# Optimization experiments

Measured on AMD Instinct MI355X. Metric: run time of the kernel, lower is better.

## Reference

```python
import jax, jax.numpy as jnp
import numpy as np

EPS = 1e-06


def _feature_map(x):
    # elu(x) + 1  (elu with alpha=1)
    return jnp.where(x > 0, x + 1.0, jnp.exp(x))


def setup_inputs() -> dict:
    key = jax.random.key(0)
    k1, k2, k3 = jax.random.split(key, 3)
    N, L, S, H, D = 4, 8192, 8192, 8, 64
    q = jax.random.normal(k1, (N, L, H, D), dtype=jnp.float32)
    k = jax.random.normal(k2, (N, S, H, D), dtype=jnp.float32)
    v = jax.random.normal(k3, (N, S, H, D), dtype=jnp.float32)
    q_mask = jnp.ones((N, L), dtype=jnp.float32)
    kv_mask = jnp.ones((N, S), dtype=jnp.float32)
    return {"q": q, "k": k, "v": v, "q_mask": q_mask, "kv_mask": kv_mask}


def reference(q, k, v, q_mask, kv_mask):
    # Linear attention with elu+1 feature map (Katharopoulos et al.)
    qf = _feature_map(q)  # [N, L, H, D]
    kf = _feature_map(k)  # [N, S, H, D]
    qf = q_mask[:, :, None, None] * qf
    kf = kv_mask[:, :, None, None] * kf
    vm = kv_mask[:, :, None, None] * v
    S = v.shape[1]
    # global KV state: [N, H, D, Dv]; v scaled by 1/S for numerical stability
    kv = jnp.einsum('nshd,nshv->nhdv', kf, vm / S)
    # normalizer: einsum('nlhd,nshd->nlh') == q . sum_s(k)
    k_sum = kf.sum(axis=1)  # [N, H, D]
    div = 1.0 / (jnp.einsum('nlhd,nhd->nlh', qf, k_sum) + EPS)
    out = S * jnp.einsum('nlhd,nhdv,nlh->nlhv', qf, kv, div)
    return out
```

## Files before the change

kernel.cpp:

```cpp
#include <hip/hip_runtime.h>
#include <math.h>


#define EPS 1e-6f

static constexpr int Nc = 4;
static constexpr int Lc = 8192;
static constexpr int Sc = 8192;
static constexpr int Hc = 8;
static constexpr int NH = Nc * Hc;
static constexpr int STATE = 64 * 64 + 64;
static constexpr int TS = 32;
static constexpr int TSP = 36;
static constexpr int QSP = 68;

typedef __attribute__((ext_vector_type(4))) short short4v;
typedef __attribute__((ext_vector_type(8))) short short8v;
typedef __attribute__((ext_vector_type(4))) float f32x4;

__device__ __forceinline__ float fmap(float x) {
    return x > 0.f ? x + 1.f : __expf(x);
}
__device__ __forceinline__ unsigned short f2bf(float x) {
    unsigned int u = __float_as_uint(x);
    u += 0x7FFFu + ((u >> 16) & 1u);
    return (unsigned short)(u >> 16);
}
__device__ __forceinline__ float bf2f(unsigned short h) {
    return __uint_as_float(((unsigned int)h) << 16);
}
__device__ __forceinline__ short8v ld8(const unsigned short* p) {
    short4v a = *(const short4v*)p;
    short4v b = *(const short4v*)(p + 4);
    return __builtin_shufflevector(a, b, 0, 1, 2, 3, 4, 5, 6, 7);
}
__device__ __forceinline__ unsigned int pack2(unsigned short a, unsigned short b) {
    return (unsigned)a | ((unsigned)b << 16);
}

__global__ __launch_bounds__(256, 4) void k1_partial(
    const float* __restrict__ kg, const float* __restrict__ vg,
    const float* __restrict__ kv_mask,
    float* __restrict__ partial, int chunks, int sc)
{
    __shared__ unsigned short kTh[64][TSP], kTl[64][TSP];
    __shared__ unsigned short vTh[64][TSP], vTl[64][TSP];
    __shared__ float ksb[16][64];

    const int bid = blockIdx.x;
    const int pair = bid / chunks;
    const int chunk = bid - pair * chunks;
    const int n = pair >> 3;
    const int h = pair & 7;
    const int s0 = chunk * sc;
    const int t = threadIdx.x;
    const int g = t >> 4;
    const int c4 = (t & 15) * 4;
    const int lane = t & 63;
    const int wv = t >> 6;
    const int row16 = lane & 15;
    const int g8 = (lane >> 4) * 8;

    f32x4 acc[4] = {{0.f,0.f,0.f,0.f},{0.f,0.f,0.f,0.f},
                    {0.f,0.f,0.f,0.f},{0.f,0.f,0.f,0.f}};
    float ksm[4] = {0.f, 0.f, 0.f, 0.f};

    const size_t rowstride = (size_t)Hc * 64;
    const size_t gbase = ((size_t)n * Sc * Hc + h) * 64 + c4;
    const int mbase = n * Sc;

    auto issue = [&](int sbase, float4& a0, float4& a1, float4& b0, float4& b1,
                     float& me, float& mo) {
        const int s = s0 + sbase + 2 * g;
        const size_t be = gbase + (size_t)s * rowstride;
        a0 = *(const float4*)(kg + be);
        a1 = *(const float4*)(kg + be + rowstride);
        b0 = *(const float4*)(vg + be);
        b1 = *(const float4*)(vg + be + rowstride);
        me = kv_mask[mbase + s];
        mo = kv_mask[mbase + s + 1];
    };

    auto process = [&](const float4& ck0, const float4& ck1,
                       const float4& cv0, const float4& cv1,
                       float cme, float cmo) {
        const float* kep = &ck0.x;
        const float* kop = &ck1.x;
        const float* vep = &cv0.x;
        const float* vop = &cv1.x;
        #pragma unroll
        for (int j = 0; j < 4; ++j) {
            const float fe = cme * fmap(kep[j]);
            const float fo = cmo * fmap(kop[j]);
            ksm[j] += fe + fo;
            const unsigned short he = f2bf(fe), ho = f2bf(fo);
            const unsigned short le = f2bf(fe - bf2f(he)), lo_ = f2bf(fo - bf2f(ho));
            *(unsigned int*)&kTh[c4 + j][2 * g] = pack2(he, ho);
            *(unsigned int*)&kTl[c4 + j][2 * g] = pack2(le, lo_);
            const float ue = cme * vep[j];
            const float uo = cmo * vop[j];
            const unsigned short vhe = f2bf(ue), vho = f2bf(uo);
            const unsigned short vle = f2bf(ue - bf2f(vhe)), vlo = f2bf(uo - bf2f(vho));
            *(unsigned int*)&vTh[c4 + j][2 * g] = pack2(vhe, vho);
            *(unsigned int*)&vTl[c4 + j][2 * g] = pack2(vle, vlo);
        }
        __syncthreads();

        const short8v Ah = ld8(&kTh[wv * 16 + row16][g8]);
        const short8v Al = ld8(&kTl[wv * 16 + row16][g8]);
        #pragma unroll
        for (int bt = 0; bt < 4; ++bt) {
            const short8v Bh = ld8(&vTh[bt * 16 + row16][g8]);
            const short8v Bl = ld8(&vTl[bt * 16 + row16][g8]);
            acc[bt] = __builtin_amdgcn_mfma_f32_16x16x32_bf16(Ah, Bh, acc[bt], 0, 0, 0);
            acc[bt] = __builtin_amdgcn_mfma_f32_16x16x32_bf16(Al, Bh, acc[bt], 0, 0, 0);
            acc[bt] = __builtin_amdgcn_mfma_f32_16x16x32_bf16(Ah, Bl, acc[bt], 0, 0, 0);
        }
        __syncthreads();
    };

    float4 ka0, ka1, va0, va1, kb0, kb1, vb0, vb1;
    float mea, moa, meb, mob;

    issue(0, ka0, ka1, va0, va1, mea, moa);
    for (int sb = 0; sb < sc; sb += 2 * TS) {
        issue(sb + TS, kb0, kb1, vb0, vb1, meb, mob);
        process(ka0, ka1, va0, va1, mea, moa);
        const int na = (sb + 2 * TS < sc) ? sb + 2 * TS : sb;
        issue(na, ka0, ka1, va0, va1, mea, moa);
        process(kb0, kb1, vb0, vb1, meb, mob);
    }

    float* outp = partial + (size_t)bid * STATE;
    float (*outs)[QSP] = reinterpret_cast<float (*)[QSP]>(&kTh[0][0]);
    #pragma unroll
    for (int bt = 0; bt < 4; ++bt) {
        #pragma unroll
        for (int r = 0; r < 4; ++r) {
            const int row = wv * 16 + (lane >> 4) * 4 + r;
            outs[row][bt * 16 + row16] = acc[bt][r];
        }
    }
    __syncthreads();
    #pragma unroll
    for (int p = 0; p < 4; ++p) {
        const int f = t + p * 256;
        const int row = f >> 4;
        const int cc = (f & 15) * 4;
        *(float4*)(outp + row * 64 + cc) = *(const float4*)&outs[row][cc];
    }

    *(f32x4*)&ksb[g][c4] = (f32x4){ksm[0], ksm[1], ksm[2], ksm[3]};
    __syncthreads();
    if (t < 64) {
        float s = 0.f;
        #pragma unroll
        for (int i = 0; i < 16; ++i) s += ksb[i][t];
        outp[4096 + t] = s;
    }
}

__global__ __launch_bounds__(256) void k2c_reduce_finalize(
    const float* __restrict__ src, float* __restrict__ dst, int nred)
{
    const int b = blockIdx.x;
    const int pair = b >> 1;
    const int sub = b & 1;
    const int t = threadIdx.x;
    const int ep = sub * 256 + t;
    const int d0 = (ep >> 4) * 2;
    const int c4 = (ep & 15) * 4;

    const float* sbase = src + (size_t)pair * nred * STATE;
    f32x4 a0 = {0.f,0.f,0.f,0.f}, a1 = {0.f,0.f,0.f,0.f};
    #pragma unroll 4
    for (int j = 0; j < nred; ++j) {
        const float* pj = sbase + (size_t)j * STATE;
        a0 += *(const f32x4*)(pj + (size_t)d0 * 64 + c4);
        a1 += *(const f32x4*)(pj + (size_t)(d0 + 1) * 64 + c4);
    }

    unsigned int* dw = (unsigned int*)(dst + (size_t)pair * STATE);
    #pragma unroll
    for (int i = 0; i < 4; ++i) {
        const int w = (c4 + i) * 32 + (d0 >> 1);
        const unsigned short h0 = f2bf(a0[i]), h1 = f2bf(a1[i]);
        dw[w] = pack2(h0, h1);
        dw[2048 + w] = pack2(f2bf(a0[i] - bf2f(h0)), f2bf(a1[i] - bf2f(h1)));
    }

    if (sub == 0 && t < 16) {
        f32x4 a = {0.f,0.f,0.f,0.f};
        #pragma unroll 4
        for (int j = 0; j < nred; ++j)
            a += *(const f32x4*)(sbase + (size_t)j * STATE + 4096 + t * 4);
        *(f32x4*)(dst + (size_t)pair * STATE + 4096 + t * 4) = a;
    }
}

__global__ __launch_bounds__(256, 4) void k3_out(
    const float* __restrict__ qg, const float* __restrict__ state,
    const float* __restrict__ q_mask, float* __restrict__ outg)
{
    __shared__ __align__(16) unsigned short qsp[2][64][QSP];
    __shared__ unsigned short kvt[2][64][QSP];
    __shared__ float ksum[64];
    __shared__ float dinv[64];

    const int nblk = 64;
    const int bid = blockIdx.x;
    const int pair = bid / nblk;
    const int lb = (bid - pair * nblk) * 2;
    const int n = pair >> 3;
    const int h = pair & 7;
    const int t = threadIdx.x;
    const int lane = t & 63;
    const int wv = t >> 6;
    const int row16 = lane & 15;
    const int g8 = (lane >> 4) * 8;

    const unsigned int* sw = (const unsigned int*)(state + (size_t)pair * STATE);
    #pragma unroll
    for (int i = 0; i < 8; ++i) {
        const int w = t + i * 256;
        const int dv = w >> 5;
        const int d2 = (w & 31) * 2;
        *(unsigned int*)&kvt[0][dv][d2] = sw[w];
        *(unsigned int*)&kvt[1][dv][d2] = sw[2048 + w];
    }
    if (t < 64) ksum[t] = ((const float*)state)[(size_t)pair * STATE + 4096 + t];
    __syncthreads();

    for (int tl = 0; tl < 2; ++tl) {
        const int l0 = (lb + tl) * 64;

        #pragma unroll
        for (int p = 0; p < 4; ++p) {
            const int f = t + p * 256;
            const int row = f >> 4;
            const int c4 = (f & 15) * 4;
            const int l = l0 + row;
            const size_t base = ((size_t)(n * Lc + l) * Hc + h) * 64 + c4;
            const float4 qq = *(const float4*)(qg + base);
            const float m = q_mask[n * Lc + l];
            const float q0 = m * fmap(qq.x), q1 = m * fmap(qq.y);
            const float q2 = m * fmap(qq.z), q3 = m * fmap(qq.w);
            const unsigned short h0 = f2bf(q0), h1 = f2bf(q1), h2 = f2bf(q2), h3 = f2bf(q3);
            *(unsigned int*)&qsp[0][row][c4]     = pack2(h0, h1);
            *(unsigned int*)&qsp[0][row][c4 + 2] = pack2(h2, h3);
            *(unsigned int*)&qsp[1][row][c4]     = pack2(f2bf(q0 - bf2f(h0)), f2bf(q1 - bf2f(h1)));
            *(unsigned int*)&qsp[1][row][c4 + 2] = pack2(f2bf(q2 - bf2f(h2)), f2bf(q3 - bf2f(h3)));
            float dp = q0 * ksum[c4] + q1 * ksum[c4 + 1] + q2 * ksum[c4 + 2] + q3 * ksum[c4 + 3];
            dp += __shfl_xor(dp, 1);
            dp += __shfl_xor(dp, 2);
            dp += __shfl_xor(dp, 4);
            dp += __shfl_xor(dp, 8);
            if ((t & 15) == 0) dinv[row] = 1.0f / (dp + EPS);
        }
        __syncthreads();

        f32x4 acc[4] = {{0.f,0.f,0.f,0.f},{0.f,0.f,0.f,0.f},
                        {0.f,0.f,0.f,0.f},{0.f,0.f,0.f,0.f}};
        #pragma unroll
        for (int ks = 0; ks < 2; ++ks) {
            const short8v Ah = ld8(&qsp[0][wv * 16 + row16][ks * 32 + g8]);
            const short8v Al = ld8(&qsp[1][wv * 16 + row16][ks * 32 + g8]);
            #pragma unroll
            for (int bt = 0; bt < 4; ++bt) {
                const short8v Bh = ld8(&kvt[0][bt * 16 + row16][ks * 32 + g8]);
                const short8v Bl = ld8(&kvt[1][bt * 16 + row16][ks * 32 + g8]);
                acc[bt] = __builtin_amdgcn_mfma_f32_16x16x32_bf16(Ah, Bh, acc[bt], 0, 0, 0);
                acc[bt] = __builtin_amdgcn_mfma_f32_16x16x32_bf16(Al, Bh, acc[bt], 0, 0, 0);
                acc[bt] = __builtin_amdgcn_mfma_f32_16x16x32_bf16(Ah, Bl, acc[bt], 0, 0, 0);
            }
        }
        __syncthreads();

        float (*outs)[QSP] = reinterpret_cast<float (*)[QSP]>(&qsp[0][0][0]);
        #pragma unroll
        for (int bt = 0; bt < 4; ++bt) {
            #pragma unroll
            for (int r = 0; r < 4; ++r) {
                const int row = wv * 16 + (lane >> 4) * 4 + r;
                outs[row][bt * 16 + row16] = acc[bt][r] * dinv[row];
            }
        }
        __syncthreads();

        #pragma unroll
        for (int p = 0; p < 4; ++p) {
            const int f = t + p * 256;
            const int row = f >> 4;
            const int c4 = (f & 15) * 4;
            const size_t base = ((size_t)(n * Lc + l0 + row) * Hc + h) * 64 + c4;
            *(float4*)(outg + base) = *(const float4*)&outs[row][c4];
        }
        __syncthreads();
    }
}

extern "C" void kernel_launch(void* const* d_in, const int* in_sizes, int n_in,
                              void* d_out, int out_size, void* d_ws, size_t ws_size,
                              hipStream_t stream)
{
    (void)in_sizes; (void)n_in; (void)out_size;
    const float* q       = (const float*)d_in[0];
    const float* k       = (const float*)d_in[1];
    const float* v       = (const float*)d_in[2];
    const float* q_mask  = (const float*)d_in[3];
    const float* kv_mask = (const float*)d_in[4];
    float* out = (float*)d_out;

    const size_t stBytes  = (size_t)STATE * sizeof(float);
    const size_t finBytes = (size_t)NH * stBytes;

    float* fin = (float*)d_ws;
    float* p1  = (float*)((char*)d_ws + finBytes);

    int chunks = 0;
    for (int c = 32; c >= 8; c >>= 1) {
        if (ws_size >= finBytes + (size_t)NH * c * stBytes) { chunks = c; break; }
    }

    if (chunks >= 8) {
        k1_partial<<<NH * chunks, 256, 0, stream>>>(k, v, kv_mask, p1, chunks, Sc / chunks);
        k2c_reduce_finalize<<<NH * 2, 256, 0, stream>>>(p1, fin, chunks);
    } else {
        k1_partial<<<NH, 256, 0, stream>>>(k, v, kv_mask, p1, 1, Sc);
        k2c_reduce_finalize<<<NH * 2, 256, 0, stream>>>(p1, fin, 1);
    }

    k3_out<<<NH * 64, 256, 0, stream>>>(q, fin, q_mask, out);
}
```

Measured before the change: 74.70 us.

## Warp-specialize k1 into producer and MFMA consumer waves with double-buffered LDS

Splits the k1_partial block into 512 threads: four producer waves load K/V, apply the feature map and write split-bf16 tiles into one of two LDS buffers, while four consumer waves run MFMAs on the other buffer. The aim is to overlap global loads and conversion with matrix math, where before all waves did both serially between barriers. In exchange the block is larger, uses twice the shared memory, and issues 4 blocks per CU of 512 threads, which may cut occupancy or raise register pressure.

```diff
diff --git a/kernel.cpp b/kernel.cpp
--- a/kernel.cpp
+++ b/kernel.cpp
@@ -13,6 +13,8 @@
 static constexpr int TS = 32;
 static constexpr int TSP = 36;
 static constexpr int QSP = 68;
+static constexpr int ARRB = 64 * TSP * 2;
+static constexpr int BUFB = 4 * ARRB;
 
 typedef __attribute__((ext_vector_type(4))) short short4v;
 typedef __attribute__((ext_vector_type(8))) short short8v;
@@ -38,14 +40,17 @@
     return (unsigned)a | ((unsigned)b << 16);
 }
 
-__global__ __launch_bounds__(256, 4) void k1_partial(
+struct K1Tile {
+    float4 k0, k1, v0, v1;
+    float m0, m1;
+};
+
+__global__ __launch_bounds__(512, 4) void k1_partial(
     const float* __restrict__ kg, const float* __restrict__ vg,
     const float* __restrict__ kv_mask,
     float* __restrict__ partial, int chunks, int sc)
 {
-    __shared__ unsigned short kTh[64][TSP], kTl[64][TSP];
-    __shared__ unsigned short vTh[64][TSP], vTl[64][TSP];
-    __shared__ float ksb[16][64];
+    __shared__ __align__(16) unsigned char smem[2 * BUFB];
 
     const int bid = blockIdx.x;
     const int pair = bid / chunks;
@@ -54,10 +59,12 @@
     const int h = pair & 7;
     const int s0 = chunk * sc;
     const int t = threadIdx.x;
+    const int lane = t & 63;
+    const int wv = t >> 6;
+    const bool producer = (wv < 4);
     const int g = t >> 4;
     const int c4 = (t & 15) * 4;
-    const int lane = t & 63;
-    const int wv = t >> 6;
+    const int cw = wv - 4;
     const int row16 = lane & 15;
     const int g8 = (lane >> 4) * 8;
 
@@ -69,94 +76,111 @@
     const size_t gbase = ((size_t)n * Sc * Hc + h) * 64 + c4;
     const int mbase = n * Sc;
 
-    auto issue = [&](int sbase, float4& a0, float4& a1, float4& b0, float4& b1,
-                     float& me, float& mo) {
-        const int s = s0 + sbase + 2 * g;
+    auto issue = [&](int tile, K1Tile& T) {
+        const int s = s0 + tile * TS + 2 * g;
         const size_t be = gbase + (size_t)s * rowstride;
-        a0 = *(const float4*)(kg + be);
-        a1 = *(const float4*)(kg + be + rowstride);
-        b0 = *(const float4*)(vg + be);
-        b1 = *(const float4*)(vg + be + rowstride);
-        me = kv_mask[mbase + s];
-        mo = kv_mask[mbase + s + 1];
+        T.k0 = *(const float4*)(kg + be);
+        T.k1 = *(const float4*)(kg + be + rowstride);
+        T.v0 = *(const float4*)(vg + be);
+        T.v1 = *(const float4*)(vg + be + rowstride);
+        T.m0 = kv_mask[mbase + s];
+        T.m1 = kv_mask[mbase + s + 1];
     };
 
-    auto process = [&](const float4& ck0, const float4& ck1,
-                       const float4& cv0, const float4& cv1,
-                       float cme, float cmo) {
-        const float* kep = &ck0.x;
-        const float* kop = &ck1.x;
-        const float* vep = &cv0.x;
-        const float* vop = &cv1.x;
+    auto convert = [&](const K1Tile& T, int b) {
+        unsigned char* base = smem + b * BUFB;
+        const float* kep = &T.k0.x;
+        const float* kop = &T.k1.x;
+        const float* vep = &T.v0.x;
+        const float* vop = &T.v1.x;
         #pragma unroll
         for (int j = 0; j < 4; ++j) {
-            const float fe = cme * fmap(kep[j]);
-            const float fo = cmo * fmap(kop[j]);
+            const int off = ((c4 + j) * TSP + 2 * g) * 2;
+            const float fe = T.m0 * fmap(kep[j]);
+            const float fo = T.m1 * fmap(kop[j]);
             ksm[j] += fe + fo;
             const unsigned short he = f2bf(fe), ho = f2bf(fo);
-            const unsigned short le = f2bf(fe - bf2f(he)), lo_ = f2bf(fo - bf2f(ho));
-            *(unsigned int*)&kTh[c4 + j][2 * g] = pack2(he, ho);
-            *(unsigned int*)&kTl[c4 + j][2 * g] = pack2(le, lo_);
-            const float ue = cme * vep[j];
-            const float uo = cmo * vop[j];
+            *(unsigned int*)(base + 0 * ARRB + off) = pack2(he, ho);
+            *(unsigned int*)(base + 1 * ARRB + off) =
+                pack2(f2bf(fe - bf2f(he)), f2bf(fo - bf2f(ho)));
+            const float ue = T.m0 * vep[j];
+            const float uo = T.m1 * vop[j];
             const unsigned short vhe = f2bf(ue), vho = f2bf(uo);
-            const unsigned short vle = f2bf(ue - bf2f(vhe)), vlo = f2bf(uo - bf2f(vho));
-            *(unsigned int*)&vTh[c4 + j][2 * g] = pack2(vhe, vho);
-            *(unsigned int*)&vTl[c4 + j][2 * g] = pack2(vle, vlo);
-        }
-        __syncthreads();
-
-        const short8v Ah = ld8(&kTh[wv * 16 + row16][g8]);
-        const short8v Al = ld8(&kTl[wv * 16 + row16][g8]);
+            *(unsigned int*)(base + 2 * ARRB + off) = pack2(vhe, vho);
+            *(unsigned int*)(base + 3 * ARRB + off) =
+                pack2(f2bf(ue - bf2f(vhe)), f2bf(uo - bf2f(vho)));
+        }
+    };
+
+    auto mfma_buf = [&](int b) {
+        const unsigned short* kh = (const unsigned short*)(smem + b * BUFB + 0 * ARRB);
+        const unsigned short* kl = (const unsigned short*)(smem + b * BUFB + 1 * ARRB);
+        const unsigned short* vh = (const unsigned short*)(smem + b * BUFB + 2 * ARRB);
+        const unsigned short* vl = (const unsigned short*)(smem + b * BUFB + 3 * ARRB);
+        const int arow = (cw * 16 + row16) * TSP + g8;
+        const short8v Ah = ld8(kh + arow);
+        const short8v Al = ld8(kl + arow);
         #pragma unroll
         for (int bt = 0; bt < 4; ++bt) {
-            const short8v Bh = ld8(&vTh[bt * 16 + row16][g8]);
-            const short8v Bl = ld8(&vTl[bt * 16 + row16][g8]);
+            const int brow = (bt * 16 + row16) * TSP + g8;
+            const short8v Bh = ld8(vh + brow);
+            const short8v Bl = ld8(vl + brow);
             acc[bt] = __builtin_amdgcn_mfma_f32_16x16x32_bf16(Ah, Bh, acc[bt], 0, 0, 0);
             acc[bt] = __builtin_amdgcn_mfma_f32_16x16x32_bf16(Al, Bh, acc[bt], 0, 0, 0);
             acc[bt] = __builtin_amdgcn_mfma_f32_16x16x32_bf16(Ah, Bl, acc[bt], 0, 0, 0);
         }
-        __syncthreads();
     };
 
-    float4 ka0, ka1, va0, va1, kb0, kb1, vb0, vb1;
-    float mea, moa, meb, mob;
-
-    issue(0, ka0, ka1, va0, va1, mea, moa);
-    for (int sb = 0; sb < sc; sb += 2 * TS) {
-        issue(sb + TS, kb0, kb1, vb0, vb1, meb, mob);
-        process(ka0, ka1, va0, va1, mea, moa);
-        const int na = (sb + 2 * TS < sc) ? sb + 2 * TS : sb;
-        issue(na, ka0, ka1, va0, va1, mea, moa);
-        process(kb0, kb1, vb0, vb1, meb, mob);
-    }
+    const int NT = sc / TS;
+    K1Tile A, B;
+    if (producer) issue(0, A);
+
+    for (int tt = 0; tt < NT; tt += 2) {
+        if (producer) {
+            issue(tt + 1, B);
+            convert(A, 0);
+        } else if (tt >= 1) {
+            mfma_buf(1);
+        }
+        __syncthreads();
+        if (producer) {
+            const int nx = (tt + 2 < NT) ? tt + 2 : tt + 1;
+            issue(nx, A);
+            convert(B, 1);
+        } else {
+            mfma_buf(0);
+        }
+        __syncthreads();
+    }
+    if (!producer) mfma_buf(1);
+    __syncthreads();
 
     float* outp = partial + (size_t)bid * STATE;
-    float (*outs)[QSP] = reinterpret_cast<float (*)[QSP]>(&kTh[0][0]);
+    float (*outs)[QSP] = reinterpret_cast<float (*)[QSP]>(smem);
+    float* ksb = reinterpret_cast<float*>(smem + BUFB);
+    if (!producer) {
+        #pragma unroll
+        for (int bt = 0; bt < 4; ++bt)
+            #pragma unroll
+            for (int r = 0; r < 4; ++r)
+                outs[cw * 16 + (lane >> 4) * 4 + r][bt * 16 + row16] = acc[bt][r];
+    } else {
+        *(f32x4*)&ksb[g * 64 + c4] = (f32x4){ksm[0], ksm[1], ksm[2], ksm[3]};
+    }
+    __syncthreads();
+
+    if (t < 64) {
+        float s = 0.f;
+        #pragma unroll
+        for (int i = 0; i < 16; ++i) s += ksb[i * 64 + t];
+        outp[4096 + t] = s;
+    }
     #pragma unroll
-    for (int bt = 0; bt < 4; ++bt) {
-        #pragma unroll
-        for (int r = 0; r < 4; ++r) {
-            const int row = wv * 16 + (lane >> 4) * 4 + r;
-            outs[row][bt * 16 + row16] = acc[bt][r];
-        }
-    }
-    __syncthreads();
-    #pragma unroll
-    for (int p = 0; p < 4; ++p) {
-        const int f = t + p * 256;
+    for (int p = 0; p < 2; ++p) {
+        const int f = t + p * 512;
         const int row = f >> 4;
         const int cc = (f & 15) * 4;
         *(float4*)(outp + row * 64 + cc) = *(const float4*)&outs[row][cc];
-    }
-
-    *(f32x4*)&ksb[g][c4] = (f32x4){ksm[0], ksm[1], ksm[2], ksm[3]};
-    __syncthreads();
-    if (t < 64) {
-        float s = 0.f;
-        #pragma unroll
-        for (int i = 0; i < 16; ++i) s += ksb[i][t];
-        outp[4096 + t] = s;
     }
 }
 
@@ -323,10 +347,10 @@
     }
 
     if (chunks >= 8) {
-        k1_partial<<<NH * chunks, 256, 0, stream>>>(k, v, kv_mask, p1, chunks, Sc / chunks);
+        k1_partial<<<NH * chunks, 512, 0, stream>>>(k, v, kv_mask, p1, chunks, Sc / chunks);
         k2c_reduce_finalize<<<NH * 2, 256, 0, stream>>>(p1, fin, chunks);
     } else {
-        k1_partial<<<NH, 256, 0, stream>>>(k, v, kv_mask, p1, 1, Sc);
+        k1_partial<<<NH, 512, 0, stream>>>(k, v, kv_mask, p1, 1, Sc);
         k2c_reduce_finalize<<<NH * 2, 256, 0, stream>>>(p1, fin, 1);
     }
 
```

After: 74.75 us. No clear change (+0.1%).
